# Optimization experiments

Measured on AMD Instinct MI355X. Metric: run time of the kernel, lower is better.

## Reference

```python
import jax, jax.numpy as jnp
import numpy as np

M2PI = 2.0 * np.pi


def setup_inputs() -> dict:
    key = jax.random.key(0)
    k1, k2, k3 = jax.random.split(key, 3)
    queries = jax.random.uniform(k1, (8192, 3), dtype=jnp.float32)
    keys = jax.random.uniform(k2, (8192, 3), dtype=jnp.float32)
    values = jax.random.normal(k3, (8192, 8), dtype=jnp.float32)
    kernelLen = jnp.ones((1,), dtype=jnp.float32)
    return {"queries": queries, "keys": keys, "values": values, "kernelLen": kernelLen}


def reference(queries, keys, values, kernelLen):
    # pairwise Euclidean distance via the expansion ||q-k||^2 = |q|^2 + |k|^2 - 2 q.k
    q_sq = jnp.sum(queries * queries, axis=-1)  # [N]
    k_sq = jnp.sum(keys * keys, axis=-1)        # [M]
    d2 = q_sq[:, None] + k_sq[None, :] - 2.0 * (queries @ keys.T)  # [N, M]
    cdist = jnp.sqrt(jnp.maximum(d2, 0.0)) / kernelLen  # broadcast scalar length
    c2pi = cdist * M2PI
    kernel = (2.0 + jnp.cos(c2pi)) * (1.0 - cdist) / 3.0 + jnp.sin(c2pi) / M2PI
    kernel = jnp.where(kernel > 0.0, kernel, 0.0)  # kernel * (kernel > 0)
    num = kernel @ values                     # [N, k]
    den = kernel @ jnp.ones_like(values)      # [N, k] (row-sums broadcast over k)
    return num / den + 1e-06
```

## Files before the change

### kernel.cpp

```cpp
#include <hip/hip_runtime.h>


typedef _Float16 h8 __attribute__((ext_vector_type(8)));
typedef float f32x16 __attribute__((ext_vector_type(16)));
typedef float f32x4 __attribute__((ext_vector_type(4)));

#define NCH 8
#define TPB 512
#define QPB 256
#define KSB 256
#define NTILE (KSB / 32)
#define LUTN 4096

__device__ __forceinline__ float nw_weight_exact(float cd) {
    float r  = __builtin_amdgcn_fractf(cd);
    float sn = __builtin_amdgcn_sinf(r);
    float cs = __builtin_amdgcn_cosf(r);
    float t  = (1.0f - cd) * (1.0f / 3.0f);
    float wt = fmaf(sn, 0.15915494309189535f, fmaf(cs, t, t + t));
    return fmaxf(wt, 0.0f);
}

__device__ __forceinline__ void split16(float x, _Float16& h, _Float16& l) {
    h = (_Float16)x;
    l = (_Float16)(x - (float)h);
}

__global__ __launch_bounds__(256) void nw_prep(const float* __restrict__ k,
                                               const float* __restrict__ v,
                                               const float* __restrict__ kl,
                                               h8* __restrict__ kfrag,
                                               h8* __restrict__ vfrag,
                                               int M) {
    const int idx = blockIdx.x * 256 + threadIdx.x;
    const float iL = 1.0f / kl[0];
    const float ssL = iL * iL * (float)LUTN;
    if (idx < M) {
        const float x = k[(size_t)idx * 3 + 0];
        const float y = k[(size_t)idx * 3 + 1];
        const float z = k[(size_t)idx * 3 + 2];
        const float cx = -2.0f * ssL * x, cy = -2.0f * ssL * y, cz = -2.0f * ssL * z;
        const float k2 = ssL * fmaf(x, x, fmaf(y, y, z * z));
        _Float16 cxh, cxl, cyh, cyl, czh, czl, k2h, k2l;
        split16(cx, cxh, cxl); split16(cy, cyh, cyl);
        split16(cz, czh, czl); split16(k2, k2h, k2l);
        h8 lo = {cxh, cxh, cxl, cyh, cyh, cyl, czh, czh};
        h8 hi = {czl, k2h, k2l, (_Float16)1.0f, (_Float16)1.0f,
                 (_Float16)0.0f, (_Float16)0.0f, (_Float16)0.0f};
        kfrag[idx * 2 + 0] = lo;
        kfrag[idx * 2 + 1] = hi;
    }
    const int nv = (M / 32) * 128;
    if (idx < nv) {
        const int t = idx >> 7, r = idx & 127;
        const int set = r >> 6, l = r & 63;
        const int ch = l & 31, g = l >> 5;
        h8 o;
#pragma unroll
        for (int j = 0; j < 8; ++j) {
            const int key = t * 32 + set * 16 + ((j & 3) + 8 * (j >> 2) + 4 * g);
            const float val = (ch < 8) ? v[(size_t)key * 8 + ch]
                                       : (ch == 8 ? 1.0f : 0.0f);
            o[j] = (_Float16)val;
        }
        vfrag[(size_t)(t * 2 + set) * 64 + l] = o;
    }
}

__global__ __launch_bounds__(TPB) void nw_main(const float* __restrict__ q,
                                               const h8* __restrict__ kfrag,
                                               const h8* __restrict__ vfrag,
                                               const float* __restrict__ kl,
                                               float* __restrict__ part,
                                               int N) {
    __shared__ float lutw[LUTN + 1];

    const int tid  = threadIdx.x;
    const int lane = tid & 63;
    const int wid  = tid >> 6;
    const int qg   = blockIdx.x;
    const int sb   = blockIdx.y;

    const float iL = 1.0f / kl[0];
    const float ssL = iL * iL * (float)LUTN;

    for (int e = tid; e <= LUTN; e += TPB)
        lutw[e] = nw_weight_exact(__builtin_amdgcn_sqrtf((float)e * (1.0f / (float)LUTN)));
    __syncthreads();

    const int row = lane & 31;
    const int g   = lane >> 5;
    const int qi  = qg * QPB + wid * 32 + row;
    const float qx = q[qi * 3 + 0];
    const float qy = q[qi * 3 + 1];
    const float qz = q[qi * 3 + 2];
    const float q2 = ssL * fmaf(qx, qx, fmaf(qy, qy, qz * qz)) + 0.5f;

    _Float16 qxh, qxl, qyh, qyl, qzh, qzl, q2h, q2l;
    split16(qx, qxh, qxl); split16(qy, qyh, qyl);
    split16(qz, qzh, qzl); split16(q2, q2h, q2l);
    const _Float16 one = (_Float16)1.0f, zer = (_Float16)0.0f;
    h8 qf;
    qf[0] = g ? qzh : qxh;
    qf[1] = g ? one : qxl;
    qf[2] = g ? one : qxh;
    qf[3] = g ? q2h : qyh;
    qf[4] = g ? q2l : qyl;
    qf[5] = g ? zer : qyh;
    qf[6] = g ? zer : qzh;
    qf[7] = g ? zer : qzl;

    const h8* __restrict__ kfq = kfrag + (size_t)(sb * KSB) * 2;
    const h8* __restrict__ vfq = vfrag + (size_t)(sb * NTILE) * 128;

    f32x16 acc;
#pragma unroll
    for (int e = 0; e < 16; ++e) acc[e] = 0.0f;
    f32x16 zacc;
#pragma unroll
    for (int e = 0; e < 16; ++e) zacc[e] = 0.0f;

    for (int t = 0; t < NTILE; ++t) {
        const h8 ka  = kfq[(size_t)(t * 32 + row) * 2 + g];
        const h8 vfa = vfq[(size_t)(t * 2 + 0) * 64 + lane];
        const h8 vfb = vfq[(size_t)(t * 2 + 1) * 64 + lane];

        const f32x16 s = __builtin_amdgcn_mfma_f32_32x32x16_f16(ka, qf, zacc, 0, 0, 0);

        h8 afa, afb;
#pragma unroll
        for (int r = 0; r < 8; ++r) {
            float fx = fmaxf(fminf(s[r], (float)LUTN), 0.0f);
            afa[r] = (_Float16)lutw[(unsigned)fx];
        }
#pragma unroll
        for (int r = 0; r < 8; ++r) {
            float fx = fmaxf(fminf(s[8 + r], (float)LUTN), 0.0f);
            afb[r] = (_Float16)lutw[(unsigned)fx];
        }
        acc = __builtin_amdgcn_mfma_f32_32x32x16_f16(afa, vfa, acc, 0, 0, 0);
        acc = __builtin_amdgcn_mfma_f32_32x32x16_f16(afb, vfb, acc, 0, 0, 0);
    }

    const int ch = lane & 31;
    if (ch < 9) {
#pragma unroll
        for (int rq = 0; rq < 4; ++rq) {
            f32x4 o = {acc[4 * rq + 0], acc[4 * rq + 1], acc[4 * rq + 2], acc[4 * rq + 3]};
            const int gi = qg * QPB + wid * 32 + 8 * rq + 4 * g;
            *(f32x4*)(part + ((size_t)sb * 10 + ch) * N + gi) = o;
        }
    }
}

__global__ __launch_bounds__(256) void nw_reduce(const float* __restrict__ part,
                                                 float* __restrict__ out,
                                                 int N, int nsb) {
    const int i = blockIdx.x * 256 + threadIdx.x;
    if (i >= N) return;
    float o[NCH];
#pragma unroll
    for (int c = 0; c < NCH; ++c) o[c] = 0.0f;
    float den = 0.0f;
    for (int sb = 0; sb < nsb; ++sb) {
        const float* base = part + (size_t)sb * 10 * N + i;
        den += base[8 * (size_t)N];
#pragma unroll
        for (int c = 0; c < NCH; ++c) o[c] += base[(size_t)c * N];
    }
    const float rd = 1.0f / den;
    float4* o4 = (float4*)(out + (size_t)i * NCH);
    o4[0] = make_float4(fmaf(o[0], rd, 1e-6f), fmaf(o[1], rd, 1e-6f),
                        fmaf(o[2], rd, 1e-6f), fmaf(o[3], rd, 1e-6f));
    o4[1] = make_float4(fmaf(o[4], rd, 1e-6f), fmaf(o[5], rd, 1e-6f),
                        fmaf(o[6], rd, 1e-6f), fmaf(o[7], rd, 1e-6f));
}

__global__ __launch_bounds__(256) void nw_full(const float* __restrict__ q,
                                               const float* __restrict__ k,
                                               const float* __restrict__ v,
                                               const float* __restrict__ kl,
                                               float* __restrict__ out,
                                               int N, int M) {
    const int i = blockIdx.x * 256 + threadIdx.x;
    if (i >= N) return;
    const float qx = q[i * 3 + 0], qy = q[i * 3 + 1], qz = q[i * 3 + 2];
    const float invL = 1.0f / kl[0];
    float num[NCH];
#pragma unroll
    for (int c = 0; c < NCH; ++c) num[c] = 0.0f;
    float den = 0.0f;
    for (int j = 0; j < M; ++j) {
        float dx = qx - k[j * 3 + 0], dy = qy - k[j * 3 + 1], dz = qz - k[j * 3 + 2];
        float d2 = fmaf(dx, dx, fmaf(dy, dy, dz * dz));
        float wt = nw_weight_exact(__builtin_amdgcn_sqrtf(d2) * invL);
        den += wt;
#pragma unroll
        for (int c = 0; c < NCH; ++c) num[c] = fmaf(wt, v[j * NCH + c], num[c]);
    }
    const float rden = 1.0f / den;
#pragma unroll
    for (int c = 0; c < NCH; ++c) out[i * NCH + c] = fmaf(num[c], rden, 1e-6f);
}

extern "C" void kernel_launch(void* const* d_in, const int* in_sizes, int n_in,
                              void* d_out, int out_size, void* d_ws, size_t ws_size,
                              hipStream_t stream) {
    const float* q  = (const float*)d_in[0];
    const float* k  = (const float*)d_in[1];
    const float* v  = (const float*)d_in[2];
    const float* kl = (const float*)d_in[3];
    float* out = (float*)d_out;

    const int N = in_sizes[0] / 3;
    const int M = in_sizes[1] / 3;

    const int nsb = (M + KSB - 1) / KSB;
    const size_t part_sz  = (size_t)nsb * 10 * N * sizeof(float);
    const size_t kfrag_sz = (size_t)M * 2 * sizeof(h8);
    const size_t vfrag_sz = (size_t)(M / 32) * 128 * sizeof(h8);

    if ((N % QPB) == 0 && (M % KSB) == 0 && ws_size >= part_sz + kfrag_sz + vfrag_sz) {
        float* part  = (float*)d_ws;
        h8*    kfrag = (h8*)((char*)d_ws + part_sz);
        h8*    vfrag = (h8*)((char*)d_ws + part_sz + kfrag_sz);
        const int nprep = (M / 32) * 128;
        nw_prep<<<(nprep + 255) / 256, 256, 0, stream>>>(k, v, kl, kfrag, vfrag, M);
        dim3 grid(N / QPB, nsb);
        nw_main<<<grid, TPB, 0, stream>>>(q, kfrag, vfrag, kl, part, N);
        nw_reduce<<<(N + 255) / 256, 256, 0, stream>>>(part, out, N, nsb);
    } else {
        nw_full<<<(N + 255) / 256, 256, 0, stream>>>(q, k, v, kl, out, N, M);
    }
}
```

Before: 34.07 us.

## Precompute fp16 weight LUT once in prep, copy to LDS; prefetch fragments

The 4097-entry weight lookup table is now computed once in the prep kernel as fp16 and written to workspace. The main kernel copies it into shared memory with vector loads, so each block no longer evaluates sin/cos/sqrt for every entry. LDS use halves, and the block shrinks to 256 threads and 128 queries, which doubles the number of blocks. The key and value fragment loads are also software-prefetched one tile ahead; the wrapped index makes the last iteration issue a redundant load.

```diff
diff --git a/kernel.cpp b/kernel.cpp
--- a/kernel.cpp
+++ b/kernel.cpp
@@ -6,11 +6,12 @@
 typedef float f32x4 __attribute__((ext_vector_type(4)));
 
 #define NCH 8
-#define TPB 512
-#define QPB 256
+#define TPB 256
+#define QPB 128
 #define KSB 256
 #define NTILE (KSB / 32)
 #define LUTN 4096
+#define LUTPAD 4104
 
 __device__ __forceinline__ float nw_weight_exact(float cd) {
     float r  = __builtin_amdgcn_fractf(cd);
@@ -31,10 +32,16 @@
                                                const float* __restrict__ kl,
                                                h8* __restrict__ kfrag,
                                                h8* __restrict__ vfrag,
+                                               _Float16* __restrict__ lutg,
                                                int M) {
     const int idx = blockIdx.x * 256 + threadIdx.x;
     const float iL = 1.0f / kl[0];
     const float ssL = iL * iL * (float)LUTN;
+    if (idx < LUTPAD) {
+        lutg[idx] = (idx <= LUTN)
+            ? (_Float16)nw_weight_exact(__builtin_amdgcn_sqrtf((float)idx * (1.0f / (float)LUTN)))
+            : (_Float16)0.0f;
+    }
     if (idx < M) {
         const float x = k[(size_t)idx * 3 + 0];
         const float y = k[(size_t)idx * 3 + 1];
@@ -70,10 +77,12 @@
 __global__ __launch_bounds__(TPB) void nw_main(const float* __restrict__ q,
                                                const h8* __restrict__ kfrag,
                                                const h8* __restrict__ vfrag,
+                                               const _Float16* __restrict__ lutg,
                                                const float* __restrict__ kl,
                                                float* __restrict__ part,
                                                int N) {
-    __shared__ float lutw[LUTN + 1];
+    __shared__ uint4 lutbuf[LUTPAD / 8];
+    _Float16* lutw16 = (_Float16*)lutbuf;
 
     const int tid  = threadIdx.x;
     const int lane = tid & 63;
@@ -81,12 +90,14 @@
     const int qg   = blockIdx.x;
     const int sb   = blockIdx.y;
 
+    {
+        const uint4* g4 = (const uint4*)lutg;
+        for (int e = tid; e < LUTPAD / 8; e += TPB) lutbuf[e] = g4[e];
+    }
+    __syncthreads();
+
     const float iL = 1.0f / kl[0];
     const float ssL = iL * iL * (float)LUTN;
-
-    for (int e = tid; e <= LUTN; e += TPB)
-        lutw[e] = nw_weight_exact(__builtin_amdgcn_sqrtf((float)e * (1.0f / (float)LUTN)));
-    __syncthreads();
 
     const int row = lane & 31;
     const int g   = lane >> 5;
@@ -120,26 +131,34 @@
 #pragma unroll
     for (int e = 0; e < 16; ++e) zacc[e] = 0.0f;
 
+    h8 ka  = kfq[(size_t)(row) * 2 + g];
+    h8 vfa = vfq[lane];
+    h8 vfb = vfq[64 + lane];
+
+#pragma unroll 2
     for (int t = 0; t < NTILE; ++t) {
-        const h8 ka  = kfq[(size_t)(t * 32 + row) * 2 + g];
-        const h8 vfa = vfq[(size_t)(t * 2 + 0) * 64 + lane];
-        const h8 vfb = vfq[(size_t)(t * 2 + 1) * 64 + lane];
+        const int tn = (t + 1) & (NTILE - 1);
+        const h8 ka_n  = kfq[(size_t)(tn * 32 + row) * 2 + g];
+        const h8 vfa_n = vfq[(size_t)(tn * 2 + 0) * 64 + lane];
+        const h8 vfb_n = vfq[(size_t)(tn * 2 + 1) * 64 + lane];
 
         const f32x16 s = __builtin_amdgcn_mfma_f32_32x32x16_f16(ka, qf, zacc, 0, 0, 0);
 
         h8 afa, afb;
 #pragma unroll
         for (int r = 0; r < 8; ++r) {
-            float fx = fmaxf(fminf(s[r], (float)LUTN), 0.0f);
-            afa[r] = (_Float16)lutw[(unsigned)fx];
+            const float fx = fmaxf(fminf(s[r], (float)LUTN), 0.0f);
+            afa[r] = lutw16[(unsigned)fx];
         }
 #pragma unroll
         for (int r = 0; r < 8; ++r) {
-            float fx = fmaxf(fminf(s[8 + r], (float)LUTN), 0.0f);
-            afb[r] = (_Float16)lutw[(unsigned)fx];
+            const float fx = fmaxf(fminf(s[8 + r], (float)LUTN), 0.0f);
+            afb[r] = lutw16[(unsigned)fx];
         }
         acc = __builtin_amdgcn_mfma_f32_32x32x16_f16(afa, vfa, acc, 0, 0, 0);
         acc = __builtin_amdgcn_mfma_f32_32x32x16_f16(afb, vfb, acc, 0, 0, 0);
+
+        ka = ka_n; vfa = vfa_n; vfb = vfb_n;
     }
 
     const int ch = lane & 31;
@@ -219,15 +238,18 @@
     const size_t part_sz  = (size_t)nsb * 10 * N * sizeof(float);
     const size_t kfrag_sz = (size_t)M * 2 * sizeof(h8);
     const size_t vfrag_sz = (size_t)(M / 32) * 128 * sizeof(h8);
-
-    if ((N % QPB) == 0 && (M % KSB) == 0 && ws_size >= part_sz + kfrag_sz + vfrag_sz) {
-        float* part  = (float*)d_ws;
-        h8*    kfrag = (h8*)((char*)d_ws + part_sz);
-        h8*    vfrag = (h8*)((char*)d_ws + part_sz + kfrag_sz);
+    const size_t lut_sz   = (size_t)LUTPAD * sizeof(_Float16);
+
+    if ((N % QPB) == 0 && (M % KSB) == 0 &&
+        ws_size >= part_sz + kfrag_sz + vfrag_sz + lut_sz) {
+        float*    part  = (float*)d_ws;
+        h8*       kfrag = (h8*)((char*)d_ws + part_sz);
+        h8*       vfrag = (h8*)((char*)d_ws + part_sz + kfrag_sz);
+        _Float16* lutg  = (_Float16*)((char*)d_ws + part_sz + kfrag_sz + vfrag_sz);
         const int nprep = (M / 32) * 128;
-        nw_prep<<<(nprep + 255) / 256, 256, 0, stream>>>(k, v, kl, kfrag, vfrag, M);
+        nw_prep<<<(nprep + 255) / 256, 256, 0, stream>>>(k, v, kl, kfrag, vfrag, lutg, M);
         dim3 grid(N / QPB, nsb);
-        nw_main<<<grid, TPB, 0, stream>>>(q, kfrag, vfrag, kl, part, N);
+        nw_main<<<grid, TPB, 0, stream>>>(q, kfrag, vfrag, lutg, kl, part, N);
         nw_reduce<<<(N + 255) / 256, 256, 0, stream>>>(part, out, N, nsb);
     } else {
         nw_full<<<(N + 255) / 256, 256, 0, stream>>>(q, k, v, kl, out, N, M);
```

Result: slower. 43.37 us (+27.3%).
